# Performance work log

Measured on AMD Instinct MI355X. Metric: run time of the kernel, lower is better.

## Reference

```python
import jax, jax.numpy as jnp
import numpy as np

DIM, HEADS, WH, WW, NPROMPT, NW, BATCH = 384, 12, 7, 7, 5, 64, 32
N = WH * WW + NPROMPT  # 54


def _make_rel_index():
    ch, cw = np.meshgrid(np.arange(WH), np.arange(WW), indexing='ij')
    coords = np.stack([ch, cw]).reshape(2, -1)  # [2, 49]
    rel = coords[:, :, None] - coords[:, None, :]  # [2,49,49]
    rel = rel.transpose(1, 2, 0)
    rel[:, :, 0] += WH - 1
    rel[:, :, 1] += WW - 1
    rel[:, :, 0] *= 2 * WW - 1
    return rel.sum(-1).astype(np.int32)  # [49,49]


def setup_inputs() -> dict:
    key = jax.random.key(0)
    ks = jax.random.split(key, 7)
    B_ = BATCH * NW
    x = jax.random.normal(ks[0], (B_, N, DIM), jnp.float32)
    # 0/-inf style shifted-window mask; random floats exercise the same math
    mask = jnp.where(jax.random.uniform(ks[1], (NW, WH * WW, WH * WW)) > 0.8,
                     jnp.float32(-100.0), jnp.float32(0.0))
    qkv_w = 0.02 * jax.random.normal(ks[2], (3 * DIM, DIM), jnp.float32)
    qkv_b = 0.02 * jax.random.normal(ks[3], (3 * DIM,), jnp.float32)
    proj_w = 0.02 * jax.random.normal(ks[4], (DIM, DIM), jnp.float32)
    proj_b = 0.02 * jax.random.normal(ks[5], (DIM,), jnp.float32)
    rpb_table = 0.02 * jax.random.normal(ks[6], ((2 * WH - 1) * (2 * WW - 1), HEADS), jnp.float32)
    rel_index = jnp.asarray(_make_rel_index())
    return {"x": x, "mask": mask, "qkv_w": qkv_w, "qkv_b": qkv_b,
            "proj_w": proj_w, "proj_b": proj_b, "rpb_table": rpb_table,
            "rel_index": rel_index}


def reference(x, mask, qkv_w, qkv_b, proj_w, proj_b, rpb_table, rel_index):
    B_, n, C = x.shape
    hd = C // HEADS
    scale = hd ** -0.5
    qkv = (x @ qkv_w.T + qkv_b).reshape(B_, n, 3, HEADS, hd)
    qkv = jnp.moveaxis(qkv, 2, 0)  # [3, B_, n, H, hd]
    q, k, v = qkv[0], qkv[1], qkv[2]  # [B_, n, H, hd]
    attn = jnp.einsum('bnhd,bmhd->bhnm', q * scale, k)  # [B_, H, n, n]
    nw2 = WH * WW
    bias = rpb_table[rel_index.reshape(-1)].reshape(nw2, nw2, HEADS)
    bias = jnp.transpose(bias, (2, 0, 1))  # [H, 49, 49]
    bias = jnp.pad(bias, ((0, 0), (NPROMPT, 0), (NPROMPT, 0)))  # [H, n, n]
    attn = attn + bias[None]
    nW = mask.shape[0]
    mask_p = jnp.pad(mask, ((0, 0), (NPROMPT, 0), (NPROMPT, 0)))  # [nW, n, n]
    attn = attn.reshape(B_ // nW, nW, HEADS, n, n) + mask_p[None, :, None]
    attn = jax.nn.softmax(attn.reshape(B_, HEADS, n, n), axis=-1)
    out = jnp.einsum('bhnm,bmhd->bnhd', attn, v).reshape(B_, n, C)
    return out @ proj_w.T + proj_b
```

## Files before the change

### kernel.cpp

```cpp
#include <hip/hip_runtime.h>

#define DIM 384
#define NH 12
#define NT 54
#define NWIN 64
#define MTOT 110592
#define HS ((size_t)MTOT * 32)

typedef __attribute__((ext_vector_type(8))) short short8;
typedef __attribute__((ext_vector_type(4))) float f32x4;

__device__ __forceinline__ unsigned short f2bf(float f) {
  unsigned int u = __float_as_uint(f);
  u += 0x7fffu + ((u >> 16) & 1u);
  return (unsigned short)(u >> 16);
}
__device__ __forceinline__ float bf2f(unsigned short s) {
  return __uint_as_float((unsigned int)s << 16);
}
__device__ __forceinline__ unsigned int cvtpk(float a, float b) {
  unsigned int r;
  asm("v_cvt_pk_bf16_f32 %0, %1, %2" : "=v"(r) : "v"(a), "v"(b));
  return r;
}
__device__ __forceinline__ void gload16(const unsigned short* g,
                                        unsigned short* l) {
  __builtin_amdgcn_global_load_lds(
      (const __attribute__((address_space(1))) void*)g,
      (__attribute__((address_space(3))) void*)l, 16, 0, 0);
}

__global__ __launch_bounds__(256) void convert_x(
    const float* __restrict__ x, unsigned short* __restrict__ xb) {
  const size_t i8 = ((size_t)blockIdx.x * 256 + threadIdx.x) * 8;
  float4 fa = *(const float4*)&x[i8];
  float4 fb = *(const float4*)&x[i8 + 4];
  uint4 u;
  u.x = cvtpk(fa.x, fa.y);
  u.y = cvtpk(fa.z, fa.w);
  u.z = cvtpk(fb.x, fb.y);
  u.w = cvtpk(fb.z, fb.w);
  *(uint4*)&xb[i8] = u;
}

__global__ __launch_bounds__(256) void prep2_kernel(
    const float* __restrict__ qkv_w, const float* __restrict__ proj_w,
    const float* __restrict__ mask, const float* __restrict__ rpb,
    const int* __restrict__ rel,
    unsigned short* __restrict__ Wq, unsigned short* __restrict__ Wp,
    unsigned short* __restrict__ bmt) {
  int idx = blockIdx.x * 256 + threadIdx.x;
  if (idx < 1152 * 384) { Wq[idx] = f2bf(qkv_w[idx]); return; }
  idx -= 1152 * 384;
  if (idx < 384 * 384) { Wp[idx] = f2bf(proj_w[idx]); return; }
  idx -= 384 * 384;
  if (idx < NWIN * NH * 64 * 64) {
    int w = idx / (NH * 4096);
    int rem = idx - w * (NH * 4096);
    int h = rem >> 12, r = (rem >> 6) & 63, c = rem & 63;
    float v;
    if (r >= NT || c >= NT) v = -1e30f;
    else if (r >= 5 && c >= 5)
      v = rpb[rel[(r - 5) * 49 + (c - 5)] * NH + h] +
          mask[w * 2401 + (r - 5) * 49 + (c - 5)];
    else v = 0.0f;
    bmt[w * (NH * 4096) + (h << 12) + (c << 6) + r] = f2bf(v);
  }
}

__global__ __launch_bounds__(256) void qkv_gemm5(
    const unsigned short* __restrict__ xb, const unsigned short* __restrict__ Wq,
    const float* __restrict__ qkv_b,
    unsigned short* __restrict__ Qb, unsigned short* __restrict__ Kb,
    unsigned short* __restrict__ Vb) {
  __shared__ unsigned short As[128][64];
  __shared__ unsigned short Bs[128][64];
  const int s = blockIdx.x;
  const int xcd = s & 7, slot = s >> 3;
  const size_t m0 = (size_t)(xcd * 108 + slot / 9) * 128;
  const int n0 = (slot % 9) * 128;
  const int tid = threadIdx.x;
  const int wv = tid >> 6, ln = tid & 63, g = ln >> 4, lc = ln & 15;
  const int wr = (wv >> 1) * 64, wc = (wv & 1) * 64;
  const int l7 = lc & 7;
  const int lr8 = ln >> 3;
  const int sc8 = (((ln & 7) ^ lr8) & 7) * 8;

  f32x4 acc[4][4];
#pragma unroll
  for (int i = 0; i < 4; ++i)
#pragma unroll
    for (int j = 0; j < 4; ++j) acc[i][j] = (f32x4){0.f, 0.f, 0.f, 0.f};

#pragma unroll
  for (int kc = 0; kc < 6; ++kc) {
    const int k0 = kc * 64;
    if (kc) __syncthreads();
#pragma unroll
    for (int it = 0; it < 4; ++it) {
      const int r0 = wv * 32 + it * 8;
      const int r = r0 + lr8;
      gload16(&xb[(m0 + r) * 384 + k0 + sc8], &As[r0][0]);
      gload16(&Wq[(size_t)(n0 + r) * 384 + k0 + sc8], &Bs[r0][0]);
    }
    __syncthreads();
#pragma unroll
    for (int kk = 0; kk < 2; ++kk) {
      const int cix = (((kk * 4 + g) ^ l7)) * 8;
      short8 af[4], bfv[4];
#pragma unroll
      for (int ms = 0; ms < 4; ++ms)
        af[ms] = *(const short8*)&As[wr + ms * 16 + lc][cix];
#pragma unroll
      for (int ns = 0; ns < 4; ++ns)
        bfv[ns] = *(const short8*)&Bs[wc + ns * 16 + lc][cix];
#pragma unroll
      for (int ms = 0; ms < 4; ++ms)
#pragma unroll
        for (int ns = 0; ns < 4; ++ns)
          acc[ms][ns] = __builtin_amdgcn_mfma_f32_16x16x32_bf16(
              af[ms], bfv[ns], acc[ms][ns], 0, 0, 0);
    }
  }

  const int sel = n0 / 384;
  const float factor = (sel == 0) ? 0.17677669529663687f : 1.0f;
  unsigned short* outp = (sel == 0) ? Qb : (sel == 1 ? Kb : Vb);
#pragma unroll
  for (int ns = 0; ns < 4; ++ns) {
    const int n = n0 + wc + ns * 16 + lc;
    const int rl = n - sel * 384;
    const int h = rl >> 5, d = rl & 31;
    const float bias = qkv_b[n];
#pragma unroll
    for (int ms = 0; ms < 4; ++ms) {
      const size_t mrow = m0 + wr + ms * 16 + g * 4;
      const float v0 = (acc[ms][ns][0] + bias) * factor;
      const float v1 = (acc[ms][ns][1] + bias) * factor;
      const float v2 = (acc[ms][ns][2] + bias) * factor;
      const float v3 = (acc[ms][ns][3] + bias) * factor;
      const unsigned int u01 = cvtpk(v0, v1);
      const unsigned int u23 = cvtpk(v2, v3);
      unsigned short* p = &outp[(size_t)h * HS + mrow * 32 + d];
      p[0]  = (unsigned short)(u01 & 0xffffu);
      p[32] = (unsigned short)(u01 >> 16);
      p[64] = (unsigned short)(u23 & 0xffffu);
      p[96] = (unsigned short)(u23 >> 16);
    }
  }
}

__global__ __launch_bounds__(256) void attn2_kernel(
    unsigned short* __restrict__ Qb, const unsigned short* __restrict__ Kb,
    const unsigned short* __restrict__ Vb, const unsigned short* __restrict__ bmt) {
  __shared__ unsigned short Ps[NT][72];
  __shared__ unsigned short vT[32][72];
  const int s = blockIdx.x;
  const int xcd = s & 7, r3 = s >> 3;
  const int h = r3 % 12;
  const int t2 = r3 / 12;
  const int batch = t2 & 31;
  const int w = xcd * 8 + (t2 >> 5);
  const int b = batch * 64 + w;
  const int tid = threadIdx.x;
  const int wv = tid >> 6, ln = tid & 63, g = ln >> 4, lc = ln & 15;
  const int m0 = wv * 16;
  const size_t base = (size_t)b * NT;
  const int arow = (m0 + lc < NT) ? (m0 + lc) : (NT - 1);
  unsigned short* Qh = Qb + (size_t)h * HS;
  const unsigned short* Kh = Kb + (size_t)h * HS;
  const unsigned short* Vh = Vb + (size_t)h * HS;

  for (int i = tid; i < 320; i += 256) {
    int d = i / 10, m = NT + (i - d * 10);
    vT[d][m] = 0;
  }

  const int vr = tid >> 2, vc = (tid & 3) * 8;
  short8 vv;
  if (tid < 216)
    vv = *(const short8*)&Vh[(base + vr) * 32 + vc];

  short8 a = *(const short8*)&Qh[(base + arow) * 32 + g * 8];
  const unsigned short* bmh = &bmt[(size_t)(w * NH + h) << 12];
  const int row0 = m0 + g * 4;
  short8 kb[4];
  uint2 uu[4];
#pragma unroll
  for (int t = 0; t < 4; ++t) {
    const int col = t * 16 + lc;
    const int kr = (col < NT) ? col : (NT - 1);
    kb[t] = *(const short8*)&Kh[(base + kr) * 32 + g * 8];
    uu[t] = *(const uint2*)&bmh[(col << 6) + row0];
  }

  f32x4 sac[4];
#pragma unroll
  for (int t = 0; t < 4; ++t) {
    f32x4 c0;
    c0[0] = bf2f((unsigned short)(uu[t].x & 0xffffu));
    c0[1] = bf2f((unsigned short)(uu[t].x >> 16));
    c0[2] = bf2f((unsigned short)(uu[t].y & 0xffffu));
    c0[3] = bf2f((unsigned short)(uu[t].y >> 16));
    sac[t] = __builtin_amdgcn_mfma_f32_16x16x32_bf16(a, kb[t], c0, 0, 0, 0);
  }
  float rmax[4] = {-3.0e38f, -3.0e38f, -3.0e38f, -3.0e38f};
#pragma unroll
  for (int t = 0; t < 4; ++t)
#pragma unroll
    for (int rr = 0; rr < 4; ++rr) rmax[rr] = fmaxf(rmax[rr], sac[t][rr]);
#pragma unroll
  for (int rr = 0; rr < 4; ++rr)
#pragma unroll
    for (int off = 1; off < 16; off <<= 1)
      rmax[rr] = fmaxf(rmax[rr], __shfl_xor(rmax[rr], off));
  float rsum[4] = {0.f, 0.f, 0.f, 0.f};
#pragma unroll
  for (int t = 0; t < 4; ++t)
#pragma unroll
    for (int rr = 0; rr < 4; ++rr) {
      float p = __expf(sac[t][rr] - rmax[rr]);
      sac[t][rr] = p;
      rsum[rr] += p;
    }
#pragma unroll
  for (int rr = 0; rr < 4; ++rr) {
#pragma unroll
    for (int off = 1; off < 16; off <<= 1)
      rsum[rr] += __shfl_xor(rsum[rr], off);
    rsum[rr] = 1.0f / rsum[rr];
  }
#pragma unroll
  for (int t = 0; t < 4; ++t) {
    const int col = t * 16 + lc;
    const unsigned int u01 = cvtpk(sac[t][0] * rsum[0], sac[t][1] * rsum[1]);
    const unsigned int u23 = cvtpk(sac[t][2] * rsum[2], sac[t][3] * rsum[3]);
    if (row0 < NT)     Ps[row0][col]     = (unsigned short)(u01 & 0xffffu);
    if (row0 + 1 < NT) Ps[row0 + 1][col] = (unsigned short)(u01 >> 16);
    if (row0 + 2 < NT) Ps[row0 + 2][col] = (unsigned short)(u23 & 0xffffu);
    if (row0 + 3 < NT) Ps[row0 + 3][col] = (unsigned short)(u23 >> 16);
  }
  if (tid < 216) {
#pragma unroll
    for (int j = 0; j < 8; ++j) vT[vc + j][vr] = (unsigned short)vv[j];
  }
  __syncthreads();
  f32x4 oac[2];
  oac[0] = (f32x4){0.f, 0.f, 0.f, 0.f};
  oac[1] = (f32x4){0.f, 0.f, 0.f, 0.f};
#pragma unroll
  for (int k2 = 0; k2 < 2; ++k2) {
    short8 pa = *(const short8*)&Ps[arow][k2 * 32 + g * 8];
#pragma unroll
    for (int tn = 0; tn < 2; ++tn) {
      short8 vb = *(const short8*)&vT[tn * 16 + lc][k2 * 32 + g * 8];
      oac[tn] = __builtin_amdgcn_mfma_f32_16x16x32_bf16(pa, vb, oac[tn], 0, 0, 0);
    }
  }
#pragma unroll
  for (int tn = 0; tn < 2; ++tn) {
    const int d = tn * 16 + lc;
    const unsigned int u01 = cvtpk(oac[tn][0], oac[tn][1]);
    const unsigned int u23 = cvtpk(oac[tn][2], oac[tn][3]);
    unsigned short* p = &Qh[(base + row0) * 32 + d];
    if (row0 < NT)     p[0]  = (unsigned short)(u01 & 0xffffu);
    if (row0 + 1 < NT) p[32] = (unsigned short)(u01 >> 16);
    if (row0 + 2 < NT) p[64] = (unsigned short)(u23 & 0xffffu);
    if (row0 + 3 < NT) p[96] = (unsigned short)(u23 >> 16);
  }
}

__global__ __launch_bounds__(256) void proj_hmajor(
    const unsigned short* __restrict__ AO, const unsigned short* __restrict__ Wp,
    const float* __restrict__ proj_b, float* __restrict__ out) {
  __shared__ unsigned short As[128][72];
  __shared__ unsigned short Bs[128][72];
  const int s = blockIdx.x;
  const int xcd = s & 7, slot = s >> 3;
  const size_t m0 = (size_t)(xcd * 108 + slot / 3) * 128;
  const int n0 = (slot % 3) * 128;
  const int tid = threadIdx.x;
  const int wv = tid >> 6, ln = tid & 63, g = ln >> 4, lc = ln & 15;
  const int wr = (wv >> 1) * 64, wc = (wv & 1) * 64;
  f32x4 acc[4][4];
#pragma unroll
  for (int i = 0; i < 4; ++i)
#pragma unroll
    for (int j = 0; j < 4; ++j) acc[i][j] = (f32x4){0.f, 0.f, 0.f, 0.f};

  const int srow = tid >> 3, l8 = tid & 7;
  for (int kc = 0; kc < 6; ++kc) {
    const int k0 = kc * 64;
    const int kg = k0 + l8 * 8;
    const int hh = kg >> 5, dd = kg & 31;
#pragma unroll
    for (int it = 0; it < 4; ++it) {
      const int r = srow + it * 32;
      *(short8*)&As[r][l8 * 8] =
          *(const short8*)&AO[(size_t)hh * HS + (m0 + r) * 32 + dd];
      *(short8*)&Bs[r][l8 * 8] =
          *(const short8*)&Wp[(size_t)(n0 + r) * 384 + kg];
    }
    __syncthreads();
#pragma unroll
    for (int kk = 0; kk < 2; ++kk) {
      short8 af[4], bfv[4];
#pragma unroll
      for (int ms = 0; ms < 4; ++ms)
        af[ms] = *(const short8*)&As[wr + ms * 16 + lc][kk * 32 + g * 8];
#pragma unroll
      for (int ns = 0; ns < 4; ++ns)
        bfv[ns] = *(const short8*)&Bs[wc + ns * 16 + lc][kk * 32 + g * 8];
#pragma unroll
      for (int ms = 0; ms < 4; ++ms)
#pragma unroll
        for (int ns = 0; ns < 4; ++ns)
          acc[ms][ns] = __builtin_amdgcn_mfma_f32_16x16x32_bf16(
              af[ms], bfv[ns], acc[ms][ns], 0, 0, 0);
    }
    __syncthreads();
  }
#pragma unroll
  for (int ns = 0; ns < 4; ++ns) {
    const int n = n0 + wc + ns * 16 + lc;
    const float pb = proj_b[n];
#pragma unroll
    for (int ms = 0; ms < 4; ++ms)
#pragma unroll
      for (int rr = 0; rr < 4; ++rr) {
        const size_t m = m0 + wr + ms * 16 + g * 4 + rr;
        out[m * 384 + n] = acc[ms][ns][rr] + pb;
      }
  }
}

__global__ __launch_bounds__(256) void prep_kernel(
    const float* __restrict__ qkv_w, const float* __restrict__ proj_w,
    const float* __restrict__ mask, const float* __restrict__ rpb,
    const int* __restrict__ rel,
    unsigned short* __restrict__ Wq, unsigned short* __restrict__ Wp,
    float* __restrict__ bias_tab, float* __restrict__ maskp) {
  int idx = blockIdx.x * 256 + threadIdx.x;
  if (idx < 1152 * 384) { Wq[idx] = f2bf(qkv_w[idx]); return; }
  idx -= 1152 * 384;
  if (idx < 384 * 384) { Wp[idx] = f2bf(proj_w[idx]); return; }
  idx -= 384 * 384;
  if (idx < NH * 64 * 64) {
    int h = idx >> 12, r = (idx >> 6) & 63, c = idx & 63;
    float v;
    if (r >= NT || c >= NT) v = -1e30f;
    else if (r >= 5 && c >= 5) v = rpb[rel[(r - 5) * 49 + (c - 5)] * NH + h];
    else v = 0.0f;
    bias_tab[idx] = v;
    return;
  }
  idx -= NH * 64 * 64;
  if (idx < NWIN * 64 * 64) {
    int w = idx >> 12, r = (idx >> 6) & 63, c = idx & 63;
    float v = 0.0f;
    if (r >= 5 && r < NT && c >= 5 && c < NT)
      v = mask[w * 2401 + (r - 5) * 49 + (c - 5)];
    maskp[idx] = v;
  }
}

__global__ __launch_bounds__(256) void fused_attn(
    const float* __restrict__ x, const unsigned short* __restrict__ Wq,
    const float* __restrict__ qkv_b, const float* __restrict__ bias_tab,
    const float* __restrict__ maskp, unsigned short* __restrict__ AO) {
  __shared__ unsigned short xs[NT][392];
  __shared__ unsigned short qs[NT][40];
  __shared__ unsigned short ksm[NT][40];
  __shared__ unsigned short vT[32][72];
  __shared__ unsigned short Ps[NT][72];
  const int b = blockIdx.x;
  const int tid = threadIdx.x;
  const int wv = tid >> 6, ln = tid & 63;
  const int g = ln >> 4, lc = ln & 15;
  const int m0 = wv * 16;
  const int wi = b & 63;
  const float scale = 0.17677669529663687f;
  const float* xb = x + (size_t)b * (NT * DIM);
  for (int i = tid; i < NT * DIM / 4; i += 256) {
    float4 v = ((const float4*)xb)[i];
    int e = i * 4, r = e / DIM, c = e - r * DIM;
    unsigned short* p = &xs[r][c];
    p[0] = f2bf(v.x); p[1] = f2bf(v.y); p[2] = f2bf(v.z); p[3] = f2bf(v.w);
  }
  __syncthreads();
  const int arow = (m0 + lc < NT) ? (m0 + lc) : (NT - 1);
  for (int h = 0; h < NH; ++h) {
    f32x4 acc[6];
#pragma unroll
    for (int t = 0; t < 6; ++t) acc[t] = (f32x4){0.f, 0.f, 0.f, 0.f};
#pragma unroll 2
    for (int kk = 0; kk < 12; ++kk) {
      short8 a = *(const short8*)&xs[arow][kk * 32 + g * 8];
#pragma unroll
      for (int t = 0; t < 6; ++t) {
        const int sel = t >> 1;
        const int wrow = sel * 384 + h * 32 + (t & 1) * 16 + lc;
        short8 bfr = *(const short8*)&Wq[wrow * 384 + kk * 32 + g * 8];
        acc[t] = __builtin_amdgcn_mfma_f32_16x16x32_bf16(a, bfr, acc[t], 0, 0, 0);
      }
    }
#pragma unroll
    for (int t = 0; t < 6; ++t) {
      const int sel = t >> 1;
      const int d = (t & 1) * 16 + lc;
      const float bias = qkv_b[sel * 384 + h * 32 + d];
#pragma unroll
      for (int r = 0; r < 4; ++r) {
        const int m = m0 + g * 4 + r;
        float v = acc[t][r] + bias;
        if (sel == 2) vT[d][m] = f2bf(v);
        else if (m < NT) {
          if (sel == 0) qs[m][d] = f2bf(v * scale);
          else ksm[m][d] = f2bf(v);
        }
      }
    }
    __syncthreads();
    f32x4 sac[4];
    {
      short8 a = *(const short8*)&qs[arow][g * 8];
#pragma unroll
      for (int t = 0; t < 4; ++t) {
        const int kr = (t * 16 + lc < NT) ? (t * 16 + lc) : (NT - 1);
        short8 bfr = *(const short8*)&ksm[kr][g * 8];
        sac[t] = __builtin_amdgcn_mfma_f32_16x16x32_bf16(
            a, bfr, (f32x4){0.f, 0.f, 0.f, 0.f}, 0, 0, 0);
      }
    }
    const float* bt = bias_tab + h * 4096;
    const float* mp = maskp + wi * 4096;
    float sv[4][4];
    float rmax[4];
#pragma unroll
    for (int r = 0; r < 4; ++r) rmax[r] = -3.0e38f;
#pragma unroll
    for (int t = 0; t < 4; ++t) {
      const int col = t * 16 + lc;
#pragma unroll
      for (int r = 0; r < 4; ++r) {
        const int row = m0 + g * 4 + r;
        float s2 = sac[t][r] + bt[row * 64 + col] + mp[row * 64 + col];
        sv[t][r] = s2;
        rmax[r] = fmaxf(rmax[r], s2);
      }
    }
#pragma unroll
    for (int r = 0; r < 4; ++r)
#pragma unroll
      for (int off = 1; off < 16; off <<= 1)
        rmax[r] = fmaxf(rmax[r], __shfl_xor(rmax[r], off));
    float rsum[4] = {0.f, 0.f, 0.f, 0.f};
#pragma unroll
    for (int t = 0; t < 4; ++t)
#pragma unroll
      for (int r = 0; r < 4; ++r) {
        float p = __expf(sv[t][r] - rmax[r]);
        sv[t][r] = p;
        rsum[r] += p;
      }
#pragma unroll
    for (int r = 0; r < 4; ++r) {
#pragma unroll
      for (int off = 1; off < 16; off <<= 1)
        rsum[r] += __shfl_xor(rsum[r], off);
      rsum[r] = 1.0f / rsum[r];
    }
#pragma unroll
    for (int t = 0; t < 4; ++t) {
      const int col = t * 16 + lc;
#pragma unroll
      for (int r = 0; r < 4; ++r) {
        const int row = m0 + g * 4 + r;
        if (row < NT) Ps[row][col] = f2bf(sv[t][r] * rsum[r]);
      }
    }
    __syncthreads();
    f32x4 oac[2];
    oac[0] = (f32x4){0.f, 0.f, 0.f, 0.f};
    oac[1] = (f32x4){0.f, 0.f, 0.f, 0.f};
#pragma unroll
    for (int k2 = 0; k2 < 2; ++k2) {
      short8 a = *(const short8*)&Ps[arow][k2 * 32 + g * 8];
#pragma unroll
      for (int tn = 0; tn < 2; ++tn) {
        short8 bfr = *(const short8*)&vT[tn * 16 + lc][k2 * 32 + g * 8];
        oac[tn] = __builtin_amdgcn_mfma_f32_16x16x32_bf16(a, bfr, oac[tn], 0, 0, 0);
      }
    }
    unsigned short* aob = AO + (size_t)b * (NT * DIM) + h * 32;
#pragma unroll
    for (int tn = 0; tn < 2; ++tn) {
      const int d = tn * 16 + lc;
#pragma unroll
      for (int r = 0; r < 4; ++r) {
        const int m = m0 + g * 4 + r;
        if (m < NT) aob[m * DIM + d] = f2bf(oac[tn][r]);
      }
    }
    __syncthreads();
  }
}

__global__ __launch_bounds__(256) void proj_kernel(
    const unsigned short* __restrict__ AO, const unsigned short* __restrict__ Wp,
    const float* __restrict__ proj_b, float* __restrict__ out, int lda) {
  __shared__ unsigned short As[128][72];
  __shared__ unsigned short Bs[128][72];
  const int s = blockIdx.x;
  const int xcd = s & 7, slot = s >> 3;
  const size_t m0 = (size_t)(xcd * 108 + slot / 3) * 128;
  const int n0 = (slot % 3) * 128;
  const int tid = threadIdx.x;
  const int wv = tid >> 6, ln = tid & 63, g = ln >> 4, lc = ln & 15;
  const int wr = (wv >> 1) * 64, wc = (wv & 1) * 64;
  f32x4 acc[4][4];
#pragma unroll
  for (int i = 0; i < 4; ++i)
#pragma unroll
    for (int j = 0; j < 4; ++j) acc[i][j] = (f32x4){0.f, 0.f, 0.f, 0.f};

  const int srow = tid >> 3, l8 = tid & 7;
  for (int kc = 0; kc < 6; ++kc) {
    const int k0 = kc * 64;
#pragma unroll
    for (int it = 0; it < 4; ++it) {
      const int r = srow + it * 32;
      *(short8*)&As[r][l8 * 8] =
          *(const short8*)&AO[(m0 + r) * (size_t)lda + k0 + l8 * 8];
      *(short8*)&Bs[r][l8 * 8] =
          *(const short8*)&Wp[(size_t)(n0 + r) * 384 + k0 + l8 * 8];
    }
    __syncthreads();
#pragma unroll
    for (int kk = 0; kk < 2; ++kk) {
      short8 af[4], bfr[4];
#pragma unroll
      for (int ms = 0; ms < 4; ++ms)
        af[ms] = *(const short8*)&As[wr + ms * 16 + lc][kk * 32 + g * 8];
#pragma unroll
      for (int ns = 0; ns < 4; ++ns)
        bfr[ns] = *(const short8*)&Bs[wc + ns * 16 + lc][kk * 32 + g * 8];
#pragma unroll
      for (int ms = 0; ms < 4; ++ms)
#pragma unroll
        for (int ns = 0; ns < 4; ++ns)
          acc[ms][ns] = __builtin_amdgcn_mfma_f32_16x16x32_bf16(
              af[ms], bfr[ns], acc[ms][ns], 0, 0, 0);
    }
    __syncthreads();
  }
#pragma unroll
  for (int ns = 0; ns < 4; ++ns) {
    const int n = n0 + wc + ns * 16 + lc;
    const float pb = proj_b[n];
#pragma unroll
    for (int ms = 0; ms < 4; ++ms)
#pragma unroll
      for (int rr = 0; rr < 4; ++rr) {
        const size_t m = m0 + wr + ms * 16 + g * 4 + rr;
        out[m * 384 + n] = acc[ms][ns][rr] + pb;
      }
  }
}

extern "C" void kernel_launch(void* const* d_in, const int* in_sizes, int n_in,
                              void* d_out, int out_size, void* d_ws, size_t ws_size,
                              hipStream_t stream) {
  const float* x      = (const float*)d_in[0];
  const float* mask   = (const float*)d_in[1];
  const float* qkv_w  = (const float*)d_in[2];
  const float* qkv_b  = (const float*)d_in[3];
  const float* proj_w = (const float*)d_in[4];
  const float* proj_b = (const float*)d_in[5];
  const float* rpb    = (const float*)d_in[6];
  const int*   rel    = (const int*)d_in[7];
  float* out = (float*)d_out;

  const size_t QKV_ELEMS = (size_t)3 * NH * HS;
  const size_t WQ_ELEMS = 1152 * 384, WP_ELEMS = 384 * 384;
  const size_t BMT_ELEMS = (size_t)NWIN * NH * 4096;
  const size_t need = (QKV_ELEMS + WQ_ELEMS + WP_ELEMS + BMT_ELEMS) * 2;

  if (ws_size >= need) {
    unsigned short* Qb  = (unsigned short*)d_ws;
    unsigned short* Kb  = Qb + NH * HS;
    unsigned short* Vb  = Kb + NH * HS;
    unsigned short* Wq  = Vb + NH * HS;
    unsigned short* Wp  = Wq + WQ_ELEMS;
    unsigned short* bmt = Wp + WP_ELEMS;
    unsigned short* xb = (unsigned short*)d_out;

    convert_x<<<20736, 256, 0, stream>>>(x, xb);
    prep2_kernel<<<14592, 256, 0, stream>>>(qkv_w, proj_w, mask, rpb, rel,
                                            Wq, Wp, bmt);
    qkv_gemm5<<<7776, 256, 0, stream>>>(xb, Wq, qkv_b, Qb, Kb, Vb);
    attn2_kernel<<<24576, 256, 0, stream>>>(Qb, Kb, Vb, bmt);
    proj_hmajor<<<2592, 256, 0, stream>>>(Qb, Wp, proj_b, out);
  } else {
    unsigned short* Wq = (unsigned short*)d_ws;
    unsigned short* Wp = Wq + 442368;
    float* bias_tab = (float*)(Wp + 147456);
    float* maskp = bias_tab + 12 * 64 * 64;
    unsigned short* AO = (unsigned short*)(maskp + 64 * 64 * 64);
    prep_kernel<<<3520, 256, 0, stream>>>(qkv_w, proj_w, mask, rpb, rel,
                                          Wq, Wp, bias_tab, maskp);
    fused_attn<<<2048, 256, 0, stream>>>(x, Wq, qkv_b, bias_tab, maskp, AO);
    proj_kernel<<<2592, 256, 0, stream>>>(AO, Wp, proj_b, out, 384);
  }
}
```

Measured before the change: 415.7 us.

## Write V pre-transposed from QKV GEMM and read it directly in attention

The QKV GEMM epilogue now stores V in a head/dim-major transposed layout using packed 8-byte stores. The attention kernel then loads the V operand fragments straight from global memory. This drops the shared-memory V transpose, its zero-fill and the block barrier. In exchange, V reads become strided global loads that are not 16-byte aligned, and they run past the 54-token window into neighbouring data. Those extra columns are only harmless because the matching probabilities are zero.

```diff
diff --git a/kernel.cpp b/kernel.cpp
--- a/kernel.cpp
+++ b/kernel.cpp
@@ -72,7 +72,7 @@
     const unsigned short* __restrict__ xb, const unsigned short* __restrict__ Wq,
     const float* __restrict__ qkv_b,
     unsigned short* __restrict__ Qb, unsigned short* __restrict__ Kb,
-    unsigned short* __restrict__ Vb) {
+    unsigned short* __restrict__ VT) {
   __shared__ unsigned short As[128][64];
   __shared__ unsigned short Bs[128][64];
   const int s = blockIdx.x;
@@ -125,7 +125,6 @@
 
   const int sel = n0 / 384;
   const float factor = (sel == 0) ? 0.17677669529663687f : 1.0f;
-  unsigned short* outp = (sel == 0) ? Qb : (sel == 1 ? Kb : Vb);
 #pragma unroll
   for (int ns = 0; ns < 4; ++ns) {
     const int n = n0 + wc + ns * 16 + lc;
@@ -141,20 +140,26 @@
       const float v3 = (acc[ms][ns][3] + bias) * factor;
       const unsigned int u01 = cvtpk(v0, v1);
       const unsigned int u23 = cvtpk(v2, v3);
-      unsigned short* p = &outp[(size_t)h * HS + mrow * 32 + d];
-      p[0]  = (unsigned short)(u01 & 0xffffu);
-      p[32] = (unsigned short)(u01 >> 16);
-      p[64] = (unsigned short)(u23 & 0xffffu);
-      p[96] = (unsigned short)(u23 >> 16);
-    }
-  }
-}
-
-__global__ __launch_bounds__(256) void attn2_kernel(
+      if (sel == 2) {
+        unsigned short* p = &VT[((size_t)h * 32 + d) * MTOT + mrow];
+        uint2 u2; u2.x = u01; u2.y = u23;
+        *(uint2*)p = u2;
+      } else {
+        unsigned short* outp = (sel == 0) ? Qb : Kb;
+        unsigned short* p = &outp[(size_t)h * HS + mrow * 32 + d];
+        p[0]  = (unsigned short)(u01 & 0xffffu);
+        p[32] = (unsigned short)(u01 >> 16);
+        p[64] = (unsigned short)(u23 & 0xffffu);
+        p[96] = (unsigned short)(u23 >> 16);
+      }
+    }
+  }
+}
+
+__global__ __launch_bounds__(256) void attn4_kernel(
     unsigned short* __restrict__ Qb, const unsigned short* __restrict__ Kb,
-    const unsigned short* __restrict__ Vb, const unsigned short* __restrict__ bmt) {
+    const unsigned short* __restrict__ VT, const unsigned short* __restrict__ bmt) {
   __shared__ unsigned short Ps[NT][72];
-  __shared__ unsigned short vT[32][72];
   const int s = blockIdx.x;
   const int xcd = s & 7, r3 = s >> 3;
   const int h = r3 % 12;
@@ -169,17 +174,7 @@
   const int arow = (m0 + lc < NT) ? (m0 + lc) : (NT - 1);
   unsigned short* Qh = Qb + (size_t)h * HS;
   const unsigned short* Kh = Kb + (size_t)h * HS;
-  const unsigned short* Vh = Vb + (size_t)h * HS;
-
-  for (int i = tid; i < 320; i += 256) {
-    int d = i / 10, m = NT + (i - d * 10);
-    vT[d][m] = 0;
-  }
-
-  const int vr = tid >> 2, vc = (tid & 3) * 8;
-  short8 vv;
-  if (tid < 216)
-    vv = *(const short8*)&Vh[(base + vr) * 32 + vc];
+  const unsigned short* VTh = VT + (size_t)h * 32 * MTOT;
 
   short8 a = *(const short8*)&Qh[(base + arow) * 32 + g * 8];
   const unsigned short* bmh = &bmt[(size_t)(w * NH + h) << 12];
@@ -240,11 +235,7 @@
     if (row0 + 2 < NT) Ps[row0 + 2][col] = (unsigned short)(u23 & 0xffffu);
     if (row0 + 3 < NT) Ps[row0 + 3][col] = (unsigned short)(u23 >> 16);
   }
-  if (tid < 216) {
-#pragma unroll
-    for (int j = 0; j < 8; ++j) vT[vc + j][vr] = (unsigned short)vv[j];
-  }
-  __syncthreads();
+
   f32x4 oac[2];
   oac[0] = (f32x4){0.f, 0.f, 0.f, 0.f};
   oac[1] = (f32x4){0.f, 0.f, 0.f, 0.f};
@@ -253,7 +244,8 @@
     short8 pa = *(const short8*)&Ps[arow][k2 * 32 + g * 8];
 #pragma unroll
     for (int tn = 0; tn < 2; ++tn) {
-      short8 vb = *(const short8*)&vT[tn * 16 + lc][k2 * 32 + g * 8];
+      short8 vb = *(const short8*)&VTh[(size_t)(tn * 16 + lc) * MTOT + base +
+                                       k2 * 32 + g * 8];
       oac[tn] = __builtin_amdgcn_mfma_f32_16x16x32_bf16(pa, vb, oac[tn], 0, 0, 0);
     }
   }
@@ -589,8 +581,8 @@
   if (ws_size >= need) {
     unsigned short* Qb  = (unsigned short*)d_ws;
     unsigned short* Kb  = Qb + NH * HS;
-    unsigned short* Vb  = Kb + NH * HS;
-    unsigned short* Wq  = Vb + NH * HS;
+    unsigned short* VT  = Kb + NH * HS;
+    unsigned short* Wq  = VT + NH * HS;
     unsigned short* Wp  = Wq + WQ_ELEMS;
     unsigned short* bmt = Wp + WP_ELEMS;
     unsigned short* xb = (unsigned short*)d_out;
@@ -598,8 +590,8 @@
     convert_x<<<20736, 256, 0, stream>>>(x, xb);
     prep2_kernel<<<14592, 256, 0, stream>>>(qkv_w, proj_w, mask, rpb, rel,
                                             Wq, Wp, bmt);
-    qkv_gemm5<<<7776, 256, 0, stream>>>(xb, Wq, qkv_b, Qb, Kb, Vb);
-    attn2_kernel<<<24576, 256, 0, stream>>>(Qb, Kb, Vb, bmt);
+    qkv_gemm5<<<7776, 256, 0, stream>>>(xb, Wq, qkv_b, Qb, Kb, VT);
+    attn4_kernel<<<24576, 256, 0, stream>>>(Qb, Kb, VT, bmt);
     proj_hmajor<<<2592, 256, 0, stream>>>(Qb, Wp, proj_b, out);
   } else {
     unsigned short* Wq = (unsigned short*)d_ws;
```

New measurement: 450.8 us. 1.08x slower.
